# Kernel tuning notes

Hardware: AMD Instinct MI355X
Metric: run time of the kernel (lower is better)

## Reference

```python
import jax, jax.numpy as jnp
import numpy as np

D_MODEL = 1024
D_FF = 4096
N_EXPERTS = 8
D_EXPERT = D_FF // N_EXPERTS  # 512
TOP_K = 2
LB_WEIGHT = 0.01
B, S = 4, 2048


def setup_inputs() -> dict:
    key = jax.random.key(0)
    ks = jax.random.split(key, 8)
    x = jax.random.normal(ks[0], (B, S, D_MODEL), dtype=jnp.float32)
    # per-expert FFN params stacked on expert axis
    w1 = jax.random.normal(ks[1], (N_EXPERTS, D_MODEL, D_EXPERT), dtype=jnp.float32) * (1.0 / np.sqrt(D_MODEL))
    b1 = jnp.zeros((N_EXPERTS, D_EXPERT), dtype=jnp.float32)
    w2 = jax.random.normal(ks[2], (N_EXPERTS, D_EXPERT, D_MODEL), dtype=jnp.float32) * (1.0 / np.sqrt(D_EXPERT))
    b2 = jnp.zeros((N_EXPERTS, D_MODEL), dtype=jnp.float32)
    centroids = jax.random.normal(ks[3], (N_EXPERTS, D_MODEL), dtype=jnp.float32) * 0.02
    w_route = jax.random.normal(ks[4], (N_EXPERTS, D_MODEL), dtype=jnp.float32) * (1.0 / np.sqrt(D_MODEL))
    return {"x": x, "w1": w1, "b1": b1, "w2": w2, "b2": b2,
            "centroids": centroids, "w_route": w_route}


def _top_k_softmax(logits, k):
    # softmax restricted to the top-k logits per token; zeros elsewhere
    vals, _ = jax.lax.top_k(logits, k)          # (..., k)
    thresh = vals[..., -1:]                     # kth-largest value
    masked = jnp.where(logits >= thresh, logits, -jnp.inf)
    return jax.nn.softmax(masked, axis=-1)


def reference(x, w1, b1, w2, b2, centroids, w_route):
    eps = 1e-12
    x_norm = x / jnp.maximum(jnp.linalg.norm(x, axis=-1, keepdims=True), eps)
    c_norm = centroids / jnp.maximum(jnp.linalg.norm(centroids, axis=-1, keepdims=True), eps)
    cos_scores = jnp.einsum('bsd,ed->bse', x_norm, c_norm)
    route_scores = jnp.einsum('bsd,ed->bse', x, w_route)
    logits = cos_scores + route_scores                       # (B,S,E)
    gates = _top_k_softmax(logits, TOP_K)                    # (B,S,E)
    # all experts computed on all tokens (dense MoE, masked combine)
    h = jax.nn.gelu(jnp.einsum('bsd,edh->bseh', x, w1) + b1, approximate=False)
    expert_out = jnp.einsum('bseh,ehd->bsed', h, w2) + b2    # (B,S,E,D)
    out = jnp.einsum('bse,bsed->bsd', gates, expert_out)
    return out
```

## Files before the change

kernel.cpp:

```cpp
#include <hip/hip_runtime.h>
#include <hip/hip_bf16.h>
#include <math.h>

#define T_TOK 8192
#define DM 1024
#define DE 512
#define NE 8
#define DFF 4096

#define CO_X   0
#define CO_W1  8388608
#define CO_W2  12582912
#define CO_B1  16777216
#define CO_B2  16781312
#define CO_CE  16789504
#define CO_WR  16797696
#define CO_TOT 16805888

#define WS_GATE2 256
#define WS_B32   65792
#define WS_TOP2  262400
#define WS_TOK   295168
#define WS_AE    360704
#define WS_AG    426240
#define WS_INV   491776
#define WS_CONV  557312
#define WS_HC    34169088
#define WS_OC    50946304

typedef __attribute__((ext_vector_type(8))) __bf16 bf16x8;
typedef __attribute__((ext_vector_type(4))) __bf16 bf16x4;
typedef __attribute__((ext_vector_type(4))) float f32x4;

__device__ __forceinline__ f32x4 ld4(const void* p, size_t off, int md)
{
  f32x4 r;
  if (md){
    bf16x4 v = *(const bf16x4*)((const __bf16*)p + off);
    #pragma unroll
    for (int j = 0; j < 4; j++) r[j] = (float)v[j];
  } else {
    r = *(const f32x4*)((const float*)p + off);
  }
  return r;
}

__device__ __forceinline__ void async_ld16(const __bf16* g, __bf16* l)
{
  __builtin_amdgcn_global_load_lds(
      (const __attribute__((address_space(1))) unsigned int*)g,
      (__attribute__((address_space(3))) unsigned int*)l, 16, 0, 0);
}

__global__ __launch_bounds__(256) void detect_k(const void* xp, const void* cp,
                                                int* meta, int* b32)
{
  const int tid = threadIdx.x;
  const float* xf = (const float*)xp;
  int ok = 0;
  for (int i = tid; i < 1024; i += 256){
    float a = fabsf(xf[i]);
    if (a > 1e-8f && a < 100.f) ok++;
  }
  __shared__ int cnt;
  __shared__ int flg;
  if (tid == 0) cnt = 0;
  __syncthreads();
  atomicAdd(&cnt, ok);
  __syncthreads();
  if (tid == 0){ flg = (cnt > 512) ? 0 : 1; meta[0] = flg; }
  __syncthreads();
  const int md = flg;

  const int e = tid >> 5, i = tid & 31;
  float ss = 0.f;
  for (int j = 0; j < 32; j++){
    size_t d = (size_t)e * DM + i + j * 32;
    float v = md ? (float)((const __bf16*)cp)[d] : ((const float*)cp)[d];
    ss += v * v;
  }
  #pragma unroll
  for (int m = 1; m < 32; m <<= 1) ss += __shfl_xor(ss, m, 64);
  float* cinv = (float*)(meta + 48);
  if (i == 0) cinv[e] = 1.f / fmaxf(sqrtf(ss), 1e-12f);

  b32[tid] = 0;
  if (tid < 8) meta[16 + tid] = 0;
}

__global__ __launch_bounds__(256) void convert_k(
    const float* __restrict__ b1, const float* __restrict__ b2,
    const float* __restrict__ ce, const float* __restrict__ wr,
    __bf16* __restrict__ dst, const int* __restrict__ meta)
{
  if (meta[0]) return;
  const size_t j = ((size_t)blockIdx.x * 256 + threadIdx.x) * 4;
  const float* src;
  const size_t doff = CO_B1 + j;
  if      (j < 4096)  src = b1 + j;
  else if (j < 12288) src = b2 + (j - 4096);
  else if (j < 20480) src = ce + (j - 12288);
  else                src = wr + (j - 20480);
  f32x4 v = *(const f32x4*)src;
  bf16x4 o;
  #pragma unroll
  for (int t = 0; t < 4; t++) o[t] = (__bf16)v[t];
  *(bf16x4*)(dst + doff) = o;
}

__global__ __launch_bounds__(256) void transp_k(
    const void* w1q, const void* w2q, __bf16* __restrict__ conv,
    const int* __restrict__ meta)
{
  const int md = meta[0];
  __shared__ __bf16 tile[32][33];
  const int b = blockIdx.x, tid = threadIdx.x;
  const int ty = tid >> 5, tx = tid & 31;

  const void* src; __bf16* dst; int ldS, ldD, i0, j0; size_t soff, doffb;
  if (b < 4096){
    const int e = b >> 9, t = b & 511;
    i0 = (t >> 4) << 5; j0 = (t & 15) << 5;
    ldS = DE; ldD = DM;
    soff = (size_t)e * DM * DE;
    dst = conv + CO_W1; doffb = (size_t)e * DE * DM;
    src = md ? (const void*)((const __bf16*)w1q) : (const void*)((const float*)w1q);
  } else {
    const int e = (b - 4096) >> 9, t = (b - 4096) & 511;
    i0 = (t >> 5) << 5; j0 = (t & 31) << 5;
    ldS = DM; ldD = DE;
    soff = (size_t)e * DE * DM;
    dst = conv + CO_W2; doffb = (size_t)e * DM * DE;
    src = md ? (const void*)((const __bf16*)w2q) : (const void*)((const float*)w2q);
  }

  #pragma unroll
  for (int rr = 0; rr < 4; rr++){
    const int r = rr * 8 + ty;
    const size_t s = soff + (size_t)(i0 + r) * ldS + j0 + tx;
    tile[r][tx] = md ? ((const __bf16*)src)[s] : (__bf16)((const float*)src)[s];
  }
  __syncthreads();
  #pragma unroll
  for (int rr = 0; rr < 4; rr++){
    const int r = rr * 8 + ty;
    dst[doffb + (size_t)(j0 + r) * ldD + i0 + tx] = tile[tx][r];
  }
}

__global__ __launch_bounds__(256) void route_k(
    const void* __restrict__ xp, const void* __restrict__ cp,
    const void* __restrict__ wp, const int* __restrict__ meta,
    __bf16* __restrict__ conv, float2* __restrict__ gate2,
    int* __restrict__ top2, int* __restrict__ b32)
{
  const int md = meta[0];
  const float* cinv = (const float*)(meta + 48);
  const int tid = threadIdx.x;
  const int g = tid >> 4, l = tid & 15;
  const int t = blockIdx.x * 16 + g;

  __shared__ int hist[8];
  if (tid < 8) hist[tid] = 0;
  __syncthreads();

  float xx = 0.f, cd[NE], wd[NE];
  #pragma unroll
  for (int e = 0; e < NE; e++){ cd[e] = 0.f; wd[e] = 0.f; }

  const size_t xbase = (size_t)t * DM;
  for (int j = 0; j < 16; j++){
    const int d0 = j * 64 + l * 4;
    f32x4 xv = ld4(xp, xbase + d0, md);
    if (!md){
      bf16x4 o;
      #pragma unroll
      for (int jj = 0; jj < 4; jj++) o[jj] = (__bf16)xv[jj];
      *(bf16x4*)(conv + CO_X + xbase + d0) = o;
    }
    xx += xv[0]*xv[0] + xv[1]*xv[1] + xv[2]*xv[2] + xv[3]*xv[3];
    #pragma unroll
    for (int e = 0; e < NE; e++){
      f32x4 cv = ld4(cp, (size_t)e * DM + d0, md);
      f32x4 wv = ld4(wp, (size_t)e * DM + d0, md);
      cd[e] += xv[0]*cv[0] + xv[1]*cv[1] + xv[2]*cv[2] + xv[3]*cv[3];
      wd[e] += xv[0]*wv[0] + xv[1]*wv[1] + xv[2]*wv[2] + xv[3]*wv[3];
    }
  }
  #pragma unroll
  for (int m = 1; m < 16; m <<= 1){
    xx += __shfl_xor(xx, m, 64);
    #pragma unroll
    for (int e = 0; e < NE; e++){
      cd[e] += __shfl_xor(cd[e], m, 64);
      wd[e] += __shfl_xor(wd[e], m, 64);
    }
  }

  if (l == 0){
    const float rxn = 1.f / fmaxf(sqrtf(xx), 1e-12f);
    float logits[NE];
    #pragma unroll
    for (int e = 0; e < NE; e++) logits[e] = cd[e] * rxn * cinv[e] + wd[e];
    float m1 = -1e30f; int i1 = 0;
    #pragma unroll
    for (int e = 0; e < NE; e++) if (logits[e] > m1){ m1 = logits[e]; i1 = e; }
    float m2 = -1e30f; int i2 = (i1 == 0) ? 1 : 0;
    #pragma unroll
    for (int e = 0; e < NE; e++)
      if (e != i1 && logits[e] > m2){ m2 = logits[e]; i2 = e; }
    float denom = 0.f, ex1 = 0.f, ex2 = 0.f;
    #pragma unroll
    for (int e = 0; e < NE; e++){
      if (logits[e] >= m2){
        float ee = expf(logits[e] - m1);
        denom += ee;
        if (e == i1) ex1 = ee;
        if (e == i2) ex2 = ee;
      }
    }
    const float inv = 1.f / denom;
    gate2[t] = make_float2(ex1 * inv, ex2 * inv);
    top2[t] = i1 | (i2 << 8);
    atomicAdd(&hist[i1], 1);
    atomicAdd(&hist[i2], 1);
  }
  __syncthreads();
  if (tid < 8) atomicAdd(&b32[(blockIdx.x >> 4) * 8 + tid], hist[tid]);
}

__global__ void offsets_k(int* meta, int* b32)
{
  const int l = threadIdx.x;
  int running = 0;
  for (int e = 0; e < NE; e++){
    int v = (l < 32) ? b32[l * 8 + e] : 0;
    int incl = v;
    #pragma unroll
    for (int ofs = 1; ofs < 32; ofs <<= 1){
      int n = __shfl_up(incl, ofs, 64);
      if (l >= ofs) incl += n;
    }
    int tot = __shfl(incl, 31, 64);
    if (l < 32) b32[l * 8 + e] = running + (incl - v);
    if (l == 0){ meta[16 + e] = tot; meta[32 + e] = running; }
    running += tot;
  }
}

__global__ __launch_bounds__(256) void place_k(
    const int* __restrict__ top2, const float2* __restrict__ gate2,
    const int* __restrict__ b32, int* __restrict__ tok, int* __restrict__ ae,
    float* __restrict__ agv, int* __restrict__ inv)
{
  __shared__ int cur[8];
  if (threadIdx.x < 8) cur[threadIdx.x] = b32[blockIdx.x * 8 + threadIdx.x];
  __syncthreads();
  const int t = blockIdx.x * 256 + threadIdx.x;
  const int p = top2[t];
  const float2 gg = gate2[t];
  const int e1 = p & 255, e2 = (p >> 8) & 255;
  const int s1 = atomicAdd(&cur[e1], 1);
  tok[s1] = t; ae[s1] = e1; agv[s1] = gg.x; inv[2 * t] = s1;
  const int s2 = atomicAdd(&cur[e2], 1);
  tok[s2] = t; ae[s2] = e2; agv[s2] = gg.y; inv[2 * t + 1] = s2;
}

__device__ __forceinline__ bool find_slot(const int* meta, int bx,
                                          int& e, int& base, int& valid)
{
  e = bx & 7;
  const int cnt = meta[16 + e];
  const int r0 = (bx >> 3) << 7;
  if (r0 >= cnt) return false;
  base = meta[32 + e] + r0;
  valid = cnt - r0;
  return true;
}

__global__ __launch_bounds__(512, 2) void gemm1g_k(
    const void* xq, const void* b1q, const __bf16* __restrict__ conv,
    const int* __restrict__ meta, const int* __restrict__ tok,
    const float* __restrict__ agv, __bf16* __restrict__ Hc)
{
  const int md = meta[0];
  const __bf16* X  = md ? (const __bf16*)xq : conv + CO_X;
  const __bf16* WT = conv + CO_W1;
  const __bf16* bb = md ? (const __bf16*)b1q : conv + CO_B1;

  int e, base, valid;
  if (!find_slot(meta, blockIdx.x, e, base, valid)) return;
  const int n0 = blockIdx.y * 256;

  __shared__ __attribute__((aligned(16))) __bf16 As[2][128 * 32];
  __shared__ __attribute__((aligned(16))) __bf16 Bs[2][256 * 32];

  const int tid = threadIdx.x;
  const int wv = tid >> 6, lane = tid & 63;
  const int q = lane >> 4, ln = lane & 15;
  const int wm = (wv >> 2) * 64, wn = (wv & 3) * 64;
  f32x4 acc[4][4] = {};

  const int sr = tid >> 2, sc = (tid & 3) * 8;
  const int ta = tok[base + ((sr < valid) ? sr : 0)];
  const __bf16* Ag  = X + (size_t)ta * DM + sc;
  const __bf16* Bg0 = WT + (size_t)e * (DE * DM) + (size_t)(n0 + sr) * DM + sc;
  const __bf16* Bg1 = Bg0 + (size_t)128 * DM;

  #define G1_STAGE(BUF, K0)                              \
    do {                                                 \
      async_ld16(Ag  + (K0), &As[BUF][tid * 8]);         \
      async_ld16(Bg0 + (K0), &Bs[BUF][tid * 8]);         \
      async_ld16(Bg1 + (K0), &Bs[BUF][tid * 8 + 4096]);  \
    } while (0)

  #define G1_COMPUTE(BUF)                                                      \
    do {                                                                       \
      bf16x8 af[4], bfr[4];                                                    \
      _Pragma("unroll")                                                        \
      for (int mi = 0; mi < 4; mi++)                                           \
        af[mi] = *(const bf16x8*)&As[BUF][(wm + mi * 16 + ln) * 32 + q * 8];   \
      _Pragma("unroll")                                                        \
      for (int ni = 0; ni < 4; ni++)                                           \
        bfr[ni] = *(const bf16x8*)&Bs[BUF][(wn + ni * 16 + ln) * 32 + q * 8];  \
      _Pragma("unroll")                                                        \
      for (int mi = 0; mi < 4; mi++)                                           \
        _Pragma("unroll")                                                      \
        for (int ni = 0; ni < 4; ni++)                                         \
          acc[mi][ni] = __builtin_amdgcn_mfma_f32_16x16x32_bf16(               \
              af[mi], bfr[ni], acc[mi][ni], 0, 0, 0);                          \
    } while (0)

  G1_STAGE(0, 0);
  __syncthreads();
  int cr = 0;
  for (int t = 0; t < 32; ++t){
    if (t < 31) G1_STAGE(cr ^ 1, (t + 1) * 32);
    G1_COMPUTE(cr);
    __syncthreads();
    cr ^= 1;
  }
  #undef G1_STAGE
  #undef G1_COMPUTE

  const int coln = n0 + wn;
  float bset[4];
  #pragma unroll
  for (int ni = 0; ni < 4; ni++)
    bset[ni] = (float)bb[e * DE + coln + ni * 16 + ln];
  #pragma unroll
  for (int mi = 0; mi < 4; mi++){
    #pragma unroll
    for (int r = 0; r < 4; r++){
      const int row = wm + mi * 16 + q * 4 + r;
      if (row < valid){
        const int slot = base + row;
        const float g = agv[slot];
        #pragma unroll
        for (int ni = 0; ni < 4; ni++){
          float v = acc[mi][ni][r] + bset[ni];
          float h = 0.5f * v * (1.0f + erff(v * 0.70710678118654752f));
          Hc[(size_t)slot * DE + coln + ni * 16 + ln] = (__bf16)(g * h);
        }
      }
    }
  }
}

__global__ __launch_bounds__(512, 2) void gemm2g_k(
    const __bf16* __restrict__ Hc, const __bf16* __restrict__ conv,
    const int* __restrict__ meta, __bf16* __restrict__ Oc)
{
  const __bf16* WT = conv + CO_W2;

  int e, base, valid;
  if (!find_slot(meta, blockIdx.x, e, base, valid)) return;
  const int n0 = blockIdx.y * 256;

  __shared__ __attribute__((aligned(16))) __bf16 As[2][128 * 32];
  __shared__ __attribute__((aligned(16))) __bf16 Bs[2][256 * 32];

  const int tid = threadIdx.x;
  const int wv = tid >> 6, lane = tid & 63;
  const int q = lane >> 4, ln = lane & 15;
  const int wm = (wv >> 2) * 64, wn = (wv & 3) * 64;
  f32x4 acc[4][4] = {};

  const int sr = tid >> 2, sc = (tid & 3) * 8;
  const int ra = (sr < valid) ? sr : 0;
  const __bf16* Ag  = Hc + (size_t)(base + ra) * DE + sc;
  const __bf16* Bg0 = WT + (size_t)e * (DM * DE) + (size_t)(n0 + sr) * DE + sc;
  const __bf16* Bg1 = Bg0 + (size_t)128 * DE;

  #define G2_STAGE(BUF, K0)                              \
    do {                                                 \
      async_ld16(Ag  + (K0), &As[BUF][tid * 8]);         \
      async_ld16(Bg0 + (K0), &Bs[BUF][tid * 8]);         \
      async_ld16(Bg1 + (K0), &Bs[BUF][tid * 8 + 4096]);  \
    } while (0)

  #define G2_COMPUTE(BUF)                                                      \
    do {                                                                       \
      bf16x8 af[4], bfr[4];                                                    \
      _Pragma("unroll")                                                        \
      for (int mi = 0; mi < 4; mi++)                                           \
        af[mi] = *(const bf16x8*)&As[BUF][(wm + mi * 16 + ln) * 32 + q * 8];   \
      _Pragma("unroll")                                                        \
      for (int ni = 0; ni < 4; ni++)                                           \
        bfr[ni] = *(const bf16x8*)&Bs[BUF][(wn + ni * 16 + ln) * 32 + q * 8];  \
      _Pragma("unroll")                                                        \
      for (int mi = 0; mi < 4; mi++)                                           \
        _Pragma("unroll")                                                      \
        for (int ni = 0; ni < 4; ni++)                                         \
          acc[mi][ni] = __builtin_amdgcn_mfma_f32_16x16x32_bf16(               \
              af[mi], bfr[ni], acc[mi][ni], 0, 0, 0);                          \
    } while (0)

  G2_STAGE(0, 0);
  __syncthreads();
  int cr = 0;
  for (int t = 0; t < 16; ++t){
    if (t < 15) G2_STAGE(cr ^ 1, (t + 1) * 32);
    G2_COMPUTE(cr);
    __syncthreads();
    cr ^= 1;
  }
  #undef G2_STAGE
  #undef G2_COMPUTE

  #pragma unroll
  for (int mi = 0; mi < 4; mi++){
    #pragma unroll
    for (int r = 0; r < 4; r++){
      const int row = wm + mi * 16 + q * 4 + r;
      if (row < valid){
        const int slot = base + row;
        #pragma unroll
        for (int ni = 0; ni < 4; ni++)
          Oc[(size_t)slot * DM + n0 + wn + ni * 16 + ln] = (__bf16)acc[mi][ni][r];
      }
    }
  }
}

__global__ __launch_bounds__(256) void combine_k(
    const __bf16* __restrict__ Oc, const int* __restrict__ inv,
    const int* __restrict__ ae, const float* __restrict__ agv,
    const void* b2q, const int* __restrict__ meta, void* out)
{
  const int md = meta[0];
  const int t = blockIdx.x;
  const int s1 = inv[2 * t], s2 = inv[2 * t + 1];
  const int e1 = ae[s1], e2 = ae[s2];
  const float g1 = agv[s1], g2 = agv[s2];
  const int c = threadIdx.x * 4;

  bf16x4 o1 = *(const bf16x4*)(Oc + (size_t)s1 * DM + c);
  bf16x4 o2 = *(const bf16x4*)(Oc + (size_t)s2 * DM + c);
  f32x4 bv1 = ld4(b2q, (size_t)e1 * DM + c, md);
  f32x4 bv2 = ld4(b2q, (size_t)e2 * DM + c, md);
  f32x4 rr;
  #pragma unroll
  for (int j = 0; j < 4; j++)
    rr[j] = (float)o1[j] + (float)o2[j] + g1 * bv1[j] + g2 * bv2[j];

  if (md){
    bf16x4 ob;
    #pragma unroll
    for (int j = 0; j < 4; j++) ob[j] = (__bf16)rr[j];
    *(bf16x4*)((__bf16*)out + (size_t)t * DM + c) = ob;
  } else {
    *(f32x4*)((float*)out + (size_t)t * DM + c) = rr;
  }
}

extern "C" void kernel_launch(void* const* d_in, const int* in_sizes, int n_in,
                              void* d_out, int out_size, void* d_ws, size_t ws_size,
                              hipStream_t stream)
{
  char* ws = (char*)d_ws;
  int*    meta  = (int*)ws;
  float2* gate2 = (float2*)(ws + WS_GATE2);
  int*    b32   = (int*)(ws + WS_B32);
  int*    top2  = (int*)(ws + WS_TOP2);
  int*    tok   = (int*)(ws + WS_TOK);
  int*    ae    = (int*)(ws + WS_AE);
  float*  agv   = (float*)(ws + WS_AG);
  int*    inv   = (int*)(ws + WS_INV);
  __bf16* conv  = (__bf16*)(ws + WS_CONV);
  __bf16* Hc    = (__bf16*)(ws + WS_HC);
  __bf16* Oc    = (__bf16*)(ws + WS_OC);

  detect_k<<<1, 256, 0, stream>>>(d_in[0], d_in[5], meta, b32);
  transp_k<<<8192, 256, 0, stream>>>(d_in[1], d_in[3], conv, meta);
  convert_k<<<28, 256, 0, stream>>>(
      (const float*)d_in[2], (const float*)d_in[4], (const float*)d_in[5],
      (const float*)d_in[6], conv, meta);
  route_k<<<T_TOK / 16, 256, 0, stream>>>(d_in[0], d_in[5], d_in[6], meta,
                                          conv, gate2, top2, b32);
  offsets_k<<<1, 64, 0, stream>>>(meta, b32);
  place_k<<<T_TOK / 256, 256, 0, stream>>>(top2, gate2, b32, tok, ae, agv, inv);
  gemm1g_k<<<dim3(512, 2), 512, 0, stream>>>(d_in[0], d_in[2], conv, meta,
                                             tok, agv, Hc);
  gemm2g_k<<<dim3(512, 4), 512, 0, stream>>>(Hc, conv, meta, Oc);
  combine_k<<<T_TOK, 256, 0, stream>>>(Oc, inv, ae, agv, d_in[4], meta, d_out);
}
```

Baseline: 251.6 us.

## Replace async global-to-LDS loads with register-staged prefetch and shrink GEMM1 N tile

Both expert GEMMs now stage the next K-slice through registers: they issue global loads before the MFMA block, then write them to the alternate LDS buffer after it. This replaces the global_load_lds async path. GEMM1's N tile is halved to 128, with half the accumulators per wave and twice the grid columns, and both kernels request 4 blocks per CU in launch bounds. The aim is more occupancy and better latency hiding, at the cost of extra VGPR traffic, LDS write instructions and possible register pressure under the tighter bound.

```diff
diff --git a/kernel.cpp b/kernel.cpp
--- a/kernel.cpp
+++ b/kernel.cpp
@@ -43,13 +43,6 @@
     r = *(const f32x4*)((const float*)p + off);
   }
   return r;
-}
-
-__device__ __forceinline__ void async_ld16(const __bf16* g, __bf16* l)
-{
-  __builtin_amdgcn_global_load_lds(
-      (const __attribute__((address_space(1))) unsigned int*)g,
-      (__attribute__((address_space(3))) unsigned int*)l, 16, 0, 0);
 }
 
 __global__ __launch_bounds__(256) void detect_k(const void* xp, const void* cp,
@@ -278,7 +271,7 @@
   return true;
 }
 
-__global__ __launch_bounds__(512, 2) void gemm1g_k(
+__global__ __launch_bounds__(512, 4) void gemm1g_k(
     const void* xq, const void* b1q, const __bf16* __restrict__ conv,
     const int* __restrict__ meta, const int* __restrict__ tok,
     const float* __restrict__ agv, __bf16* __restrict__ Hc)
@@ -290,63 +283,65 @@
 
   int e, base, valid;
   if (!find_slot(meta, blockIdx.x, e, base, valid)) return;
-  const int n0 = blockIdx.y * 256;
+  const int n0 = blockIdx.y * 128;
 
   __shared__ __attribute__((aligned(16))) __bf16 As[2][128 * 32];
-  __shared__ __attribute__((aligned(16))) __bf16 Bs[2][256 * 32];
+  __shared__ __attribute__((aligned(16))) __bf16 Bs[2][128 * 32];
 
   const int tid = threadIdx.x;
   const int wv = tid >> 6, lane = tid & 63;
   const int q = lane >> 4, ln = lane & 15;
-  const int wm = (wv >> 2) * 64, wn = (wv & 3) * 64;
-  f32x4 acc[4][4] = {};
+  const int wm = (wv >> 2) * 64, wn = (wv & 3) * 32;
+  f32x4 acc[4][2] = {};
 
   const int sr = tid >> 2, sc = (tid & 3) * 8;
   const int ta = tok[base + ((sr < valid) ? sr : 0)];
-  const __bf16* Ag  = X + (size_t)ta * DM + sc;
-  const __bf16* Bg0 = WT + (size_t)e * (DE * DM) + (size_t)(n0 + sr) * DM + sc;
-  const __bf16* Bg1 = Bg0 + (size_t)128 * DM;
-
-  #define G1_STAGE(BUF, K0)                              \
-    do {                                                 \
-      async_ld16(Ag  + (K0), &As[BUF][tid * 8]);         \
-      async_ld16(Bg0 + (K0), &Bs[BUF][tid * 8]);         \
-      async_ld16(Bg1 + (K0), &Bs[BUF][tid * 8 + 4096]);  \
-    } while (0)
+  const __bf16* Ag = X + (size_t)ta * DM + sc;
+  const __bf16* Bg = WT + (size_t)e * (DE * DM) + (size_t)(n0 + sr) * DM + sc;
 
   #define G1_COMPUTE(BUF)                                                      \
     do {                                                                       \
-      bf16x8 af[4], bfr[4];                                                    \
+      bf16x8 af[4], bfr[2];                                                    \
       _Pragma("unroll")                                                        \
       for (int mi = 0; mi < 4; mi++)                                           \
         af[mi] = *(const bf16x8*)&As[BUF][(wm + mi * 16 + ln) * 32 + q * 8];   \
       _Pragma("unroll")                                                        \
-      for (int ni = 0; ni < 4; ni++)                                           \
+      for (int ni = 0; ni < 2; ni++)                                           \
         bfr[ni] = *(const bf16x8*)&Bs[BUF][(wn + ni * 16 + ln) * 32 + q * 8];  \
       _Pragma("unroll")                                                        \
       for (int mi = 0; mi < 4; mi++)                                           \
         _Pragma("unroll")                                                      \
-        for (int ni = 0; ni < 4; ni++)                                         \
+        for (int ni = 0; ni < 2; ni++)                                         \
           acc[mi][ni] = __builtin_amdgcn_mfma_f32_16x16x32_bf16(               \
               af[mi], bfr[ni], acc[mi][ni], 0, 0, 0);                          \
     } while (0)
 
-  G1_STAGE(0, 0);
-  __syncthreads();
+  bf16x8 ra = *(const bf16x8*)Ag;
+  bf16x8 rb = *(const bf16x8*)Bg;
+  *(bf16x8*)&As[0][tid * 8] = ra;
+  *(bf16x8*)&Bs[0][tid * 8] = rb;
+  __syncthreads();
+
   int cr = 0;
   for (int t = 0; t < 32; ++t){
-    if (t < 31) G1_STAGE(cr ^ 1, (t + 1) * 32);
+    if (t < 31){
+      ra = *(const bf16x8*)(Ag + (t + 1) * 32);
+      rb = *(const bf16x8*)(Bg + (t + 1) * 32);
+    }
     G1_COMPUTE(cr);
+    if (t < 31){
+      *(bf16x8*)&As[cr ^ 1][tid * 8] = ra;
+      *(bf16x8*)&Bs[cr ^ 1][tid * 8] = rb;
+    }
     __syncthreads();
     cr ^= 1;
   }
-  #undef G1_STAGE
   #undef G1_COMPUTE
 
   const int coln = n0 + wn;
-  float bset[4];
-  #pragma unroll
-  for (int ni = 0; ni < 4; ni++)
+  float bset[2];
+  #pragma unroll
+  for (int ni = 0; ni < 2; ni++)
     bset[ni] = (float)bb[e * DE + coln + ni * 16 + ln];
   #pragma unroll
   for (int mi = 0; mi < 4; mi++){
@@ -357,7 +352,7 @@
         const int slot = base + row;
         const float g = agv[slot];
         #pragma unroll
-        for (int ni = 0; ni < 4; ni++){
+        for (int ni = 0; ni < 2; ni++){
           float v = acc[mi][ni][r] + bset[ni];
           float h = 0.5f * v * (1.0f + erff(v * 0.70710678118654752f));
           Hc[(size_t)slot * DE + coln + ni * 16 + ln] = (__bf16)(g * h);
@@ -367,7 +362,7 @@
   }
 }
 
-__global__ __launch_bounds__(512, 2) void gemm2g_k(
+__global__ __launch_bounds__(512, 4) void gemm2g_k(
     const __bf16* __restrict__ Hc, const __bf16* __restrict__ conv,
     const int* __restrict__ meta, __bf16* __restrict__ Oc)
 {
@@ -387,17 +382,10 @@
   f32x4 acc[4][4] = {};
 
   const int sr = tid >> 2, sc = (tid & 3) * 8;
-  const int ra = (sr < valid) ? sr : 0;
-  const __bf16* Ag  = Hc + (size_t)(base + ra) * DE + sc;
+  const int ra0 = (sr < valid) ? sr : 0;
+  const __bf16* Ag  = Hc + (size_t)(base + ra0) * DE + sc;
   const __bf16* Bg0 = WT + (size_t)e * (DM * DE) + (size_t)(n0 + sr) * DE + sc;
   const __bf16* Bg1 = Bg0 + (size_t)128 * DE;
-
-  #define G2_STAGE(BUF, K0)                              \
-    do {                                                 \
-      async_ld16(Ag  + (K0), &As[BUF][tid * 8]);         \
-      async_ld16(Bg0 + (K0), &Bs[BUF][tid * 8]);         \
-      async_ld16(Bg1 + (K0), &Bs[BUF][tid * 8 + 4096]);  \
-    } while (0)
 
   #define G2_COMPUTE(BUF)                                                      \
     do {                                                                       \
@@ -416,16 +404,30 @@
               af[mi], bfr[ni], acc[mi][ni], 0, 0, 0);                          \
     } while (0)
 
-  G2_STAGE(0, 0);
-  __syncthreads();
+  bf16x8 va  = *(const bf16x8*)Ag;
+  bf16x8 vb0 = *(const bf16x8*)Bg0;
+  bf16x8 vb1 = *(const bf16x8*)Bg1;
+  *(bf16x8*)&As[0][tid * 8] = va;
+  *(bf16x8*)&Bs[0][tid * 8] = vb0;
+  *(bf16x8*)&Bs[0][tid * 8 + 4096] = vb1;
+  __syncthreads();
+
   int cr = 0;
   for (int t = 0; t < 16; ++t){
-    if (t < 15) G2_STAGE(cr ^ 1, (t + 1) * 32);
+    if (t < 15){
+      va  = *(const bf16x8*)(Ag  + (t + 1) * 32);
+      vb0 = *(const bf16x8*)(Bg0 + (t + 1) * 32);
+      vb1 = *(const bf16x8*)(Bg1 + (t + 1) * 32);
+    }
     G2_COMPUTE(cr);
+    if (t < 15){
+      *(bf16x8*)&As[cr ^ 1][tid * 8] = va;
+      *(bf16x8*)&Bs[cr ^ 1][tid * 8] = vb0;
+      *(bf16x8*)&Bs[cr ^ 1][tid * 8 + 4096] = vb1;
+    }
     __syncthreads();
     cr ^= 1;
   }
-  #undef G2_STAGE
   #undef G2_COMPUTE
 
   #pragma unroll
@@ -500,7 +502,7 @@
                                           conv, gate2, top2, b32);
   offsets_k<<<1, 64, 0, stream>>>(meta, b32);
   place_k<<<T_TOK / 256, 256, 0, stream>>>(top2, gate2, b32, tok, ae, agv, inv);
-  gemm1g_k<<<dim3(512, 2), 512, 0, stream>>>(d_in[0], d_in[2], conv, meta,
+  gemm1g_k<<<dim3(512, 4), 512, 0, stream>>>(d_in[0], d_in[2], conv, meta,
                                              tok, agv, Hc);
   gemm2g_k<<<dim3(512, 4), 512, 0, stream>>>(Hc, conv, meta, Oc);
   combine_k<<<T_TOK, 256, 0, stream>>>(Oc, inv, ae, agv, d_in[4], meta, d_out);
```

After: 250.5 us. No clear change (-0.4%).
